# Performance work log

Hardware: AMD Instinct MI355X
Metric: run time of the kernel (lower is better)

Reference implementation:

```python
import jax, jax.numpy as jnp
import numpy as np

P_FACTOR = 3.0
EPS = 1e-12  # torch F.normalize eps


def _l2norm(x):
    # torch.nn.functional.normalize(x, dim=1): x / max(||x||_2, eps)
    n = jnp.sqrt(jnp.sum(x * x, axis=1, keepdims=True))
    return x / jnp.maximum(n, EPS)


def setup_inputs() -> dict:
    key = jax.random.key(0)
    k1, k2, k3, k4, k5 = jax.random.split(key, 5)
    B, N, D_IN, D_RED, C = 8192, 16384, 1024, 512, 28
    return {
        "features": jax.random.normal(k1, (B, D_IN), dtype=jnp.float32),
        "ex_features": jax.random.normal(k2, (N, D_IN), dtype=jnp.float32),
        "g_w": jax.random.normal(k3, (D_RED, D_IN), dtype=jnp.float32) * 0.02,
        "g_b": jax.random.normal(k4, (D_RED,), dtype=jnp.float32) * 0.02,
        "ex_classes": jax.random.uniform(k5, (N, C), dtype=jnp.float32),
    }


def reference(features, ex_features, g_w, g_b, ex_classes):
    # g: Linear(input_dim -> dim_reduce)
    f = features @ g_w.T + g_b          # [B, D_red]
    ef = ex_features @ g_w.T + g_b      # [N, D_red]
    # cosine similarity
    s = _l2norm(f) @ _l2norm(ef).T      # [B, N]
    # power-sign activation: |s|^p * sign(s)
    a = jnp.power(jnp.abs(s), P_FACTOR) * jnp.sign(s)
    echo = a @ ex_classes               # [B, C]
    b = jnp.clip(jnp.sum(ex_classes, axis=0), 1.0, None)
    echo = jnp.clip(echo / b, 0.0, 1.0)
    return echo
```

## Files before the change

kernel.cpp:

```cpp
#include <hip/hip_runtime.h>
#include <stdint.h>

typedef __attribute__((ext_vector_type(4))) float f32x4;
typedef __attribute__((ext_vector_type(8))) short s16x8;

#define MFMA16(A, B, C) __builtin_amdgcn_mfma_f32_16x16x32_bf16(A, B, C, 0, 0, 0)
#define WAIT_VM(N) asm volatile("s_waitcnt vmcnt(" #N ")" ::: "memory")
#define WAIT_LGKM() asm volatile("s_waitcnt lgkmcnt(0)" ::: "memory")
#define BAR() __builtin_amdgcn_s_barrier()
#define SCHED_FENCE() __builtin_amdgcn_sched_barrier(0)
#define SP1() __builtin_amdgcn_s_setprio(1)
#define SP0() __builtin_amdgcn_s_setprio(0)

#define PHASE_SYNC(N) do { SCHED_FENCE(); WAIT_LGKM(); WAIT_VM(N); BAR(); SCHED_FENCE(); } while (0)
#define PHASE_SYNC_NOVM() do { SCHED_FENCE(); WAIT_LGKM(); BAR(); SCHED_FENCE(); } while (0)

__device__ __forceinline__ unsigned short f2bf(float x) {
  union { float f; unsigned u; } v; v.f = x;
  return (unsigned short)((v.u + 0x7fffu + ((v.u >> 16) & 1u)) >> 16);
}

__global__ void k_cast_bf16(const float* __restrict__ in, unsigned short* __restrict__ out, int n4) {
  int i = blockIdx.x * blockDim.x + threadIdx.x;
  const int stride = gridDim.x * blockDim.x;
  for (; i < n4; i += stride) {
    const float4 v = ((const float4*)in)[i];
    ushort4 o;
    o.x = f2bf(v.x); o.y = f2bf(v.y); o.z = f2bf(v.z); o.w = f2bf(v.w);
    ((ushort4*)out)[i] = o;
  }
}

__global__ void k_excT(const float* __restrict__ exc, unsigned short* __restrict__ excT,
                       float* __restrict__ bvec) {
  const int c = blockIdx.x;
  const int tid = threadIdx.x;
  float sum = 0.f;
  for (int j = tid; j < 16384; j += 256) {
    const float v = (c < 28) ? exc[(size_t)j * 28 + c] : 0.f;
    excT[(size_t)c * 16384 + j] = f2bf(v);
    sum += v;
  }
  #pragma unroll
  for (int o = 32; o; o >>= 1) sum += __shfl_down(sum, o, 64);
  __shared__ float wsum[4];
  if ((tid & 63) == 0) wsum[tid >> 6] = sum;
  __syncthreads();
  if (tid == 0 && c < 28) bvec[c] = fmaxf(wsum[0] + wsum[1] + wsum[2] + wsum[3], 1.0f);
}

__device__ __forceinline__ void stage_a(const unsigned short* __restrict__ src, int ld,
                                        unsigned short* smem, int dsoff, int w, int offsrc) {
  #pragma unroll
  for (int c = 0; c < 4; ++c)
    __builtin_amdgcn_global_load_lds(
        (const __attribute__((address_space(1))) unsigned int*)(src + offsrc + c * 64 * ld),
        (__attribute__((address_space(3))) unsigned int*)(smem + dsoff + c * 4096 + w * 512),
        16, 0, 0);
}
__device__ __forceinline__ void stage_b(const unsigned short* __restrict__ src, int ld,
                                        unsigned short* smem, int dsoff, int w, int offsrc) {
  #pragma unroll
  for (int c = 0; c < 2; ++c)
    __builtin_amdgcn_global_load_lds(
        (const __attribute__((address_space(1))) unsigned int*)(src + offsrc + c * 64 * ld),
        (__attribute__((address_space(3))) unsigned int*)(smem + dsoff + c * 4096 + w * 512),
        16, 0, 0);
}

__device__ __forceinline__ void mma_step_p(const unsigned short* smem, int ao, int bo,
                                           int wr, int wc, int r, int q, f32x4 acc[8][2]) {
  const int rx = r & 7;
  #pragma unroll
  for (int ks = 0; ks < 2; ++ks) {
    const int sb = ((ks * 4 + q) ^ rx) << 3;
    s16x8 bf[2];
    #pragma unroll
    for (int j = 0; j < 2; ++j)
      bf[j] = *(const s16x8*)(smem + bo + (wc * 32 + j * 16 + r) * 64 + sb);
    #pragma unroll
    for (int i = 0; i < 8; ++i) {
      const s16x8 af = *(const s16x8*)(smem + ao + (wr * 128 + i * 16 + r) * 64 + sb);
      #pragma unroll
      for (int j = 0; j < 2; ++j)
        acc[i][j] = MFMA16(af, bf[j], acc[i][j]);
    }
  }
}

#define PA0 0
#define PB0 16384
#define PA1 24576
#define PB1 40960

__global__ __launch_bounds__(512, 2) void k_proj(const unsigned short* __restrict__ featbf,
                                                 const unsigned short* __restrict__ exbf,
                                                 const unsigned short* __restrict__ gwbf,
                                                 const float* __restrict__ gb,
                                                 float* __restrict__ fall) {
  __shared__ __align__(16) unsigned short smem[49152];
  const int tid = threadIdx.x, w = tid >> 6, lane = tid & 63;
  const int wr = w >> 2, wc = w & 3, r = lane & 15, q = lane >> 4;
  const int offsrc = (w * 8 + (lane >> 3)) * 1024 + (((lane & 7) ^ (lane >> 3)) << 3);
  const int m0 = blockIdx.x * 256;
  const int n0 = blockIdx.y * 128;
  const unsigned short* Asrc = (m0 < 8192) ? (featbf + (size_t)m0 * 1024)
                                           : (exbf + (size_t)(m0 - 8192) * 1024);
  const unsigned short* Bsrc = gwbf + (size_t)n0 * 1024;
  f32x4 acc[8][2];
  #pragma unroll
  for (int i = 0; i < 8; ++i)
    #pragma unroll
    for (int j = 0; j < 2; ++j) acc[i][j] = {0.f, 0.f, 0.f, 0.f};

  stage_a(Asrc, 1024, smem, PA0, w, offsrc);
  stage_b(Bsrc, 1024, smem, PB0, w, offsrc);
  for (int t = 0; t < 15; ++t) {
    const int na = ((t + 1) & 1) ? PA1 : PA0, nbb = ((t + 1) & 1) ? PB1 : PB0;
    stage_a(Asrc + (t + 1) * 64, 1024, smem, na, w, offsrc);
    stage_b(Bsrc + (t + 1) * 64, 1024, smem, nbb, w, offsrc);
    WAIT_VM(6);
    BAR();
    mma_step_p(smem, (t & 1) ? PA1 : PA0, (t & 1) ? PB1 : PB0, wr, wc, r, q, acc);
    WAIT_LGKM();
    BAR();
  }
  WAIT_VM(0);
  BAR();
  mma_step_p(smem, PA1, PB1, wr, wc, r, q, acc);

  #pragma unroll
  for (int j = 0; j < 2; ++j) {
    const int col = n0 + wc * 32 + j * 16 + r;
    const float bias = gb[col];
    #pragma unroll
    for (int i = 0; i < 8; ++i) {
      const int row0 = m0 + wr * 128 + i * 16 + q * 4;
      #pragma unroll
      for (int t = 0; t < 4; ++t)
        fall[(size_t)(row0 + t) * 512 + col] = acc[i][j][t] + bias;
    }
  }
}

__global__ __launch_bounds__(256) void k_norm(const float* __restrict__ fall,
                                              unsigned short* __restrict__ fn) {
  const int row = blockIdx.x * 4 + (threadIdx.x >> 6);
  const int lane = threadIdx.x & 63;
  const float4* p = (const float4*)(fall + (size_t)row * 512) + lane * 2;
  const float4 v0 = p[0], v1 = p[1];
  float ss = v0.x * v0.x + v0.y * v0.y + v0.z * v0.z + v0.w * v0.w
           + v1.x * v1.x + v1.y * v1.y + v1.z * v1.z + v1.w * v1.w;
  #pragma unroll
  for (int o = 32; o; o >>= 1) ss += __shfl_xor(ss, o, 64);
  const float sc = 1.0f / fmaxf(sqrtf(ss), 1e-12f);
  ushort4 o0, o1;
  o0.x = f2bf(v0.x * sc); o0.y = f2bf(v0.y * sc); o0.z = f2bf(v0.z * sc); o0.w = f2bf(v0.w * sc);
  o1.x = f2bf(v1.x * sc); o1.y = f2bf(v1.y * sc); o1.z = f2bf(v1.z * sc); o1.w = f2bf(v1.w * sc);
  ushort4* qo = (ushort4*)(fn + (size_t)row * 512) + lane * 2;
  qo[0] = o0; qo[1] = o1;
}

#define BUFSZ 32768
#define EXL 65536

__device__ __forceinline__ void stage_half(const unsigned short* __restrict__ src,
                                           unsigned short* smem, int dsoff, int tid) {
  const int rowh = tid >> 3;
  const unsigned short* g = src + (size_t)rowh * 512 + (((tid & 7) ^ (rowh & 7)) << 3);
  __builtin_amdgcn_global_load_lds(
      (const __attribute__((address_space(1))) unsigned int*)g,
      (__attribute__((address_space(3))) unsigned int*)(smem + dsoff + tid * 8), 16, 0, 0);
  __builtin_amdgcn_global_load_lds(
      (const __attribute__((address_space(1))) unsigned int*)(g + 64 * 512),
      (__attribute__((address_space(3))) unsigned int*)(smem + dsoff + 4096 + tid * 8), 16, 0, 0);
}

__device__ __forceinline__ void stage_exc(const unsigned short* __restrict__ excTg, int c0,
                                          unsigned short* smem, int tid) {
  const int row = tid >> 5, b = tid & 31;
  const int sb = ((b & 24) | ((b ^ (row & 7)) & 7)) << 3;
  const unsigned short* g = excTg + (size_t)row * 16384 + c0 + sb;
  __builtin_amdgcn_global_load_lds(
      (const __attribute__((address_space(1))) unsigned int*)g,
      (__attribute__((address_space(3))) unsigned int*)(smem + EXL + tid * 8), 16, 0, 0);
  __builtin_amdgcn_global_load_lds(
      (const __attribute__((address_space(1))) unsigned int*)(g + 16 * 16384),
      (__attribute__((address_space(3))) unsigned int*)(smem + EXL + 4096 + tid * 8), 16, 0, 0);
}

template<int MH, int NH>
__device__ __forceinline__ void mma_phase(const unsigned short* smem, int bufR,
                                          int wr, int wc, int r, int q, int rx,
                                          f32x4 acc[2][2][4][2]) {
  const unsigned short* A = smem + bufR + MH * 16384 + (wr * 64 + r) * 64;
  const unsigned short* B = smem + bufR + 8192 + NH * 16384 + (wc * 32 + r) * 64;
  const int s0 = (q ^ rx) << 3, s1 = ((4 + q) ^ rx) << 3;
  const s16x8 b00 = *(const s16x8*)(B + s0),        b01 = *(const s16x8*)(B + s1);
  const s16x8 b10 = *(const s16x8*)(B + 1024 + s0), b11 = *(const s16x8*)(B + 1024 + s1);
  #pragma unroll
  for (int fi = 0; fi < 4; ++fi) {
    const s16x8 a0 = *(const s16x8*)(A + fi * 1024 + s0);
    acc[MH][NH][fi][0] = MFMA16(a0, b00, acc[MH][NH][fi][0]);
    acc[MH][NH][fi][1] = MFMA16(a0, b10, acc[MH][NH][fi][1]);
    const s16x8 a1 = *(const s16x8*)(A + fi * 1024 + s1);
    acc[MH][NH][fi][0] = MFMA16(a1, b01, acc[MH][NH][fi][0]);
    acc[MH][NH][fi][1] = MFMA16(a1, b11, acc[MH][NH][fi][1]);
  }
}

__global__ __launch_bounds__(512, 2) void k_fused(const unsigned short* __restrict__ fnall,
                                                  const unsigned short* __restrict__ excT,
                                                  float* __restrict__ partial) {
  __shared__ __align__(16) unsigned short smem[73728];
  const int tid = threadIdx.x, w = tid >> 6, lane = tid & 63;
  const int wr = w >> 2, wc = w & 3, r = lane & 15, q = lane >> 4, rx = r & 7;
  const int r0 = blockIdx.x * 256;
  const int nchunk = blockIdx.y;
  const unsigned short* Abase = fnall + (size_t)r0 * 512;
  const unsigned short* Ebase = fnall + (size_t)8192 * 512;
  unsigned short* aLb = smem + BUFSZ;

  f32x4 acc[2][2][4][2];
  f32x4 eacc[2][2];
  #pragma unroll
  for (int a = 0; a < 2; ++a)
    #pragma unroll
    for (int b = 0; b < 2; ++b) eacc[a][b] = {0.f, 0.f, 0.f, 0.f};

  {
    const unsigned short* B0p = Ebase + (size_t)(nchunk * 4) * 256 * 512;
    stage_half(Abase, smem, 0, tid);
    stage_half(B0p, smem, 8192, tid);
    stage_half(Abase + 128 * 512, smem, 16384, tid);
    stage_half(B0p + 128 * 512, smem, 24576, tid);
  }

  for (int jt = 0; jt < 4; ++jt) {
    #pragma unroll
    for (int a = 0; a < 2; ++a)
      #pragma unroll
      for (int b = 0; b < 2; ++b)
        #pragma unroll
        for (int fi = 0; fi < 4; ++fi)
          #pragma unroll
          for (int fj = 0; fj < 2; ++fj) acc[a][b][fi][fj] = {0.f, 0.f, 0.f, 0.f};

    for (int tk = 0; tk < 8; ++tk) {
      const int kt = jt * 8 + tk;
      const int bufR = (kt & 1) * BUFSZ, bufW = bufR ^ BUFSZ;
      const int kn = (kt + 1) & 31;
      const unsigned short* An = Abase + (kn & 7) * 64;
      const unsigned short* Bn = Ebase + (size_t)((nchunk * 4 + (kn >> 3)) * 256) * 512 + (kn & 7) * 64;
      PHASE_SYNC(4);
      stage_half(An, smem, bufW + 0, tid);
      if (tk == 7) stage_exc(excT, (nchunk * 4 + jt) * 256, smem, tid);
      SP1(); mma_phase<0, 0>(smem, bufR, wr, wc, r, q, rx, acc); SP0();
      PHASE_SYNC(4);
      stage_half(Bn, smem, bufW + 8192, tid);
      SP1(); mma_phase<1, 0>(smem, bufR, wr, wc, r, q, rx, acc); SP0();
      PHASE_SYNC(4);
      stage_half(An + 128 * 512, smem, bufW + 16384, tid);
      SP1(); mma_phase<1, 1>(smem, bufR, wr, wc, r, q, rx, acc); SP0();
      PHASE_SYNC_NOVM();
      stage_half(Bn + 128 * 512, smem, bufW + 24576, tid);
      SP1(); mma_phase<0, 1>(smem, bufR, wr, wc, r, q, rx, acc); SP0();
    }

    const int c0 = (nchunk * 4 + jt) * 256;
    SCHED_FENCE(); WAIT_LGKM(); WAIT_VM(6); BAR(); SCHED_FENCE();
    #pragma unroll
    for (int h = 0; h < 2; ++h) {
      #pragma unroll
      for (int nh = 0; nh < 2; ++nh)
        #pragma unroll
        for (int fi = 0; fi < 4; ++fi)
          #pragma unroll
          for (int fj = 0; fj < 2; ++fj) {
            const int colc = nh * 128 + wc * 32 + fj * 16 + r;
            const int cb = colc >> 3, cl = colc & 7;
            #pragma unroll
            for (int t2 = 0; t2 < 4; ++t2) {
              const int row = wr * 64 + fi * 16 + q * 4 + t2;
              const float v = acc[h][nh][fi][fj][t2];
              aLb[row * 256 + ((((cb & 24) | ((cb ^ (row & 7)) & 7)) << 3) | cl)] = f2bf(v * v * v);
            }
          }
      SCHED_FENCE(); WAIT_LGKM(); BAR(); SCHED_FENCE();
      {
        const int rE = w * 16 + r;
        const int re8 = rE & 7;
        #pragma unroll
        for (int kc = 0; kc < 8; ++kc) {
          const int kb = kc * 4 + q;
          const s16x8 af = *(const s16x8*)(aLb + rE * 256 + (((kb & 24) | ((kb ^ re8) & 7)) << 3));
          #pragma unroll
          for (int nj = 0; nj < 2; ++nj) {
            const s16x8 bfr = *(const s16x8*)(smem + EXL + (nj * 16 + r) * 256 +
                                              (((kb & 24) | ((kb ^ rx) & 7)) << 3));
            eacc[h][nj] = MFMA16(af, bfr, eacc[h][nj]);
          }
        }
      }
      SCHED_FENCE(); WAIT_LGKM(); BAR(); SCHED_FENCE();
    }
  }

  #pragma unroll
  for (int h = 0; h < 2; ++h)
    #pragma unroll
    for (int nj = 0; nj < 2; ++nj) {
      const int rb = r0 + h * 128 + w * 16 + q * 4;
      const int cls = nj * 16 + r;
      #pragma unroll
      for (int t = 0; t < 4; ++t)
        partial[((size_t)nchunk * 8192 + rb + t) * 32 + cls] = eacc[h][nj][t];
    }
}

__global__ void k_reduce(const float* __restrict__ partial, const float* __restrict__ bvec,
                         float* __restrict__ out) {
  const int idx = blockIdx.x * 256 + threadIdx.x;
  const int row = idx / 28, c = idx - row * 28;
  float s = 0.f;
  #pragma unroll
  for (int nc = 0; nc < 16; ++nc) s += partial[((size_t)nc * 8192 + row) * 32 + c];
  out[idx] = fminf(fmaxf(s / bvec[c], 0.f), 1.f);
}

extern "C" void kernel_launch(void* const* d_in, const int* in_sizes, int n_in,
                              void* d_out, int out_size, void* d_ws, size_t ws_size,
                              hipStream_t stream) {
  const float* features    = (const float*)d_in[0];
  const float* ex_features = (const float*)d_in[1];
  const float* g_w         = (const float*)d_in[2];
  const float* g_b         = (const float*)d_in[3];
  const float* ex_classes  = (const float*)d_in[4];
  float* out = (float*)d_out;
  char* ws = (char*)d_ws;

  unsigned short* featbf = (unsigned short*)(ws + 0);
  unsigned short* exbf   = (unsigned short*)(ws + 16777216);
  unsigned short* fnall  = (unsigned short*)(ws + 0);
  float* fall            = (float*)(ws + 50331648);
  float* partial         = (float*)(ws + 50331648);
  unsigned short* gwbf   = (unsigned short*)(ws + 100663296);
  unsigned short* excT   = (unsigned short*)(ws + 101711872);
  float* bvec            = (float*)(ws + 102760448);

  k_cast_bf16<<<2048, 256, 0, stream>>>(features, featbf, 8192 * 1024 / 4);
  k_cast_bf16<<<2048, 256, 0, stream>>>(ex_features, exbf, 16384 * 1024 / 4);
  k_cast_bf16<<<512, 256, 0, stream>>>(g_w, gwbf, 512 * 1024 / 4);
  k_excT<<<32, 256, 0, stream>>>(ex_classes, excT, bvec);
  k_proj<<<dim3(96, 4), 512, 0, stream>>>(featbf, exbf, gwbf, g_b, fall);
  k_norm<<<6144, 256, 0, stream>>>(fall, fnall);
  k_fused<<<dim3(32, 16), 512, 0, stream>>>(fnall, excT, partial);
  k_reduce<<<896, 256, 0, stream>>>(partial, bvec, out);
}
```

Baseline: 255.6 us.

## Reorder MFMA quadrant phases to reuse A/B fragments across phases

Each k-step's four quadrant phases are reordered to (A0,B0), (A0,B1), (A1,B1), (A1,B0), and fragments now stay in registers between phases. This roughly halves LDS fragment reads per k-step. The async global-to-LDS staging order is permuted so each half-tile's write lands after its last read from the previous buffer. More fragment registers stay live alongside the large accumulator set, which risks spills or lower occupancy under the 512x2 launch bounds.

```diff
diff --git a/kernel.cpp b/kernel.cpp
--- a/kernel.cpp
+++ b/kernel.cpp
@@ -189,23 +189,31 @@
       (__attribute__((address_space(3))) unsigned int*)(smem + EXL + 4096 + tid * 8), 16, 0, 0);
 }
 
-template<int MH, int NH>
-__device__ __forceinline__ void mma_phase(const unsigned short* smem, int bufR,
-                                          int wr, int wc, int r, int q, int rx,
-                                          f32x4 acc[2][2][4][2]) {
+__device__ __forceinline__ void ld_a(const unsigned short* smem, int bufR, int MH,
+                                     int wr, int r, int s0, int s1, s16x8 a[4][2]) {
   const unsigned short* A = smem + bufR + MH * 16384 + (wr * 64 + r) * 64;
+  #pragma unroll
+  for (int fi = 0; fi < 4; ++fi) {
+    a[fi][0] = *(const s16x8*)(A + fi * 1024 + s0);
+    a[fi][1] = *(const s16x8*)(A + fi * 1024 + s1);
+  }
+}
+__device__ __forceinline__ void ld_b(const unsigned short* smem, int bufR, int NH,
+                                     int wc, int r, int s0, int s1, s16x8 b[2][2]) {
   const unsigned short* B = smem + bufR + 8192 + NH * 16384 + (wc * 32 + r) * 64;
-  const int s0 = (q ^ rx) << 3, s1 = ((4 + q) ^ rx) << 3;
-  const s16x8 b00 = *(const s16x8*)(B + s0),        b01 = *(const s16x8*)(B + s1);
-  const s16x8 b10 = *(const s16x8*)(B + 1024 + s0), b11 = *(const s16x8*)(B + 1024 + s1);
+  #pragma unroll
+  for (int j = 0; j < 2; ++j) {
+    b[j][0] = *(const s16x8*)(B + j * 1024 + s0);
+    b[j][1] = *(const s16x8*)(B + j * 1024 + s1);
+  }
+}
+__device__ __forceinline__ void mma_q(const s16x8 a[4][2], const s16x8 b[2][2], f32x4 accq[4][2]) {
   #pragma unroll
   for (int fi = 0; fi < 4; ++fi) {
-    const s16x8 a0 = *(const s16x8*)(A + fi * 1024 + s0);
-    acc[MH][NH][fi][0] = MFMA16(a0, b00, acc[MH][NH][fi][0]);
-    acc[MH][NH][fi][1] = MFMA16(a0, b10, acc[MH][NH][fi][1]);
-    const s16x8 a1 = *(const s16x8*)(A + fi * 1024 + s1);
-    acc[MH][NH][fi][0] = MFMA16(a1, b01, acc[MH][NH][fi][0]);
-    acc[MH][NH][fi][1] = MFMA16(a1, b11, acc[MH][NH][fi][1]);
+    accq[fi][0] = MFMA16(a[fi][0], b[0][0], accq[fi][0]);
+    accq[fi][1] = MFMA16(a[fi][0], b[1][0], accq[fi][1]);
+    accq[fi][0] = MFMA16(a[fi][1], b[0][1], accq[fi][0]);
+    accq[fi][1] = MFMA16(a[fi][1], b[1][1], accq[fi][1]);
   }
 }
 
@@ -215,6 +223,7 @@
   __shared__ __align__(16) unsigned short smem[73728];
   const int tid = threadIdx.x, w = tid >> 6, lane = tid & 63;
   const int wr = w >> 2, wc = w & 3, r = lane & 15, q = lane >> 4, rx = r & 7;
+  const int s0 = (q ^ rx) << 3, s1 = ((4 + q) ^ rx) << 3;
   const int r0 = blockIdx.x * 256;
   const int nchunk = blockIdx.y;
   const unsigned short* Abase = fnall + (size_t)r0 * 512;
@@ -232,8 +241,8 @@
     const unsigned short* B0p = Ebase + (size_t)(nchunk * 4) * 256 * 512;
     stage_half(Abase, smem, 0, tid);
     stage_half(B0p, smem, 8192, tid);
+    stage_half(B0p + 128 * 512, smem, 24576, tid);
     stage_half(Abase + 128 * 512, smem, 16384, tid);
-    stage_half(B0p + 128 * 512, smem, 24576, tid);
   }
 
   for (int jt = 0; jt < 4; ++jt) {
@@ -252,22 +261,34 @@
       const int kn = (kt + 1) & 31;
       const unsigned short* An = Abase + (kn & 7) * 64;
       const unsigned short* Bn = Ebase + (size_t)((nchunk * 4 + (kn >> 3)) * 256) * 512 + (kn & 7) * 64;
+      s16x8 afr[4][2], b0f[2][2], b1f[2][2];
       PHASE_SYNC(4);
       stage_half(An, smem, bufW + 0, tid);
       if (tk == 7) stage_exc(excT, (nchunk * 4 + jt) * 256, smem, tid);
-      SP1(); mma_phase<0, 0>(smem, bufR, wr, wc, r, q, rx, acc); SP0();
+      SP1();
+      ld_a(smem, bufR, 0, wr, r, s0, s1, afr);
+      ld_b(smem, bufR, 0, wc, r, s0, s1, b0f);
+      mma_q(afr, b0f, acc[0][0]);
+      SP0();
       PHASE_SYNC(4);
       stage_half(Bn, smem, bufW + 8192, tid);
-      SP1(); mma_phase<1, 0>(smem, bufR, wr, wc, r, q, rx, acc); SP0();
+      SP1();
+      ld_b(smem, bufR, 1, wc, r, s0, s1, b1f);
+      mma_q(afr, b1f, acc[0][1]);
+      SP0();
       PHASE_SYNC(4);
+      stage_half(Bn + 128 * 512, smem, bufW + 24576, tid);
+      SP1();
+      ld_a(smem, bufR, 1, wr, r, s0, s1, afr);
+      mma_q(afr, b1f, acc[1][1]);
+      SP0();
+      PHASE_SYNC_NOVM();
       stage_half(An + 128 * 512, smem, bufW + 16384, tid);
-      SP1(); mma_phase<1, 1>(smem, bufR, wr, wc, r, q, rx, acc); SP0();
-      PHASE_SYNC_NOVM();
-      stage_half(Bn + 128 * 512, smem, bufW + 24576, tid);
-      SP1(); mma_phase<0, 1>(smem, bufR, wr, wc, r, q, rx, acc); SP0();
-    }
-
-    const int c0 = (nchunk * 4 + jt) * 256;
+      SP1();
+      mma_q(afr, b0f, acc[1][0]);
+      SP0();
+    }
+
     SCHED_FENCE(); WAIT_LGKM(); WAIT_VM(6); BAR(); SCHED_FENCE();
     #pragma unroll
     for (int h = 0; h < 2; ++h) {
```

New measurement: 307.7 us. 20.4% more time.

## Switch main GEMM to 32x32x16 MFMA with quarter-K staging pipeline

Applied to the files above, without the earlier changes.

Replaces the 16x16x32 bf16 MFMA tiling of the similarity GEMM with 32x32x16 MFMAs, giving each wave a 128x64 sub-tile instead of split halves. The shared-memory staging is reorganized into four K-quarter stages per step, and the exc-table prefetch and next-column-chunk prefetch are peeled into a special last iteration with retuned vmcnt waits. The larger MFMA shape is meant to cut LDS read traffic per FLOP and instruction count. In exchange it drops the XOR swizzle, which risks LDS bank conflicts, and it adds more complex wait-count bookkeeping.

```diff
diff --git a/kernel.cpp b/kernel.cpp
--- a/kernel.cpp
+++ b/kernel.cpp
@@ -2,9 +2,11 @@
 #include <stdint.h>
 
 typedef __attribute__((ext_vector_type(4))) float f32x4;
+typedef __attribute__((ext_vector_type(16))) float f32x16;
 typedef __attribute__((ext_vector_type(8))) short s16x8;
 
 #define MFMA16(A, B, C) __builtin_amdgcn_mfma_f32_16x16x32_bf16(A, B, C, 0, 0, 0)
+#define MFMA32(A, B, C) __builtin_amdgcn_mfma_f32_32x32x16_bf16(A, B, C, 0, 0, 0)
 #define WAIT_VM(N) asm volatile("s_waitcnt vmcnt(" #N ")" ::: "memory")
 #define WAIT_LGKM() asm volatile("s_waitcnt lgkmcnt(0)" ::: "memory")
 #define BAR() __builtin_amdgcn_s_barrier()
@@ -13,7 +15,6 @@
 #define SP0() __builtin_amdgcn_s_setprio(0)
 
 #define PHASE_SYNC(N) do { SCHED_FENCE(); WAIT_LGKM(); WAIT_VM(N); BAR(); SCHED_FENCE(); } while (0)
-#define PHASE_SYNC_NOVM() do { SCHED_FENCE(); WAIT_LGKM(); BAR(); SCHED_FENCE(); } while (0)
 
 __device__ __forceinline__ unsigned short f2bf(float x) {
   union { float f; unsigned u; } v; v.f = x;
@@ -164,16 +165,12 @@
 #define BUFSZ 32768
 #define EXL 65536
 
-__device__ __forceinline__ void stage_half(const unsigned short* __restrict__ src,
-                                           unsigned short* smem, int dsoff, int tid) {
-  const int rowh = tid >> 3;
-  const unsigned short* g = src + (size_t)rowh * 512 + (((tid & 7) ^ (rowh & 7)) << 3);
+__device__ __forceinline__ void stage_q(const unsigned short* __restrict__ src,
+                                        unsigned short* smem, int dsoff, int tid) {
+  const unsigned short* g = src + (size_t)(tid >> 1) * 512 + (tid & 1) * 8;
   __builtin_amdgcn_global_load_lds(
       (const __attribute__((address_space(1))) unsigned int*)g,
       (__attribute__((address_space(3))) unsigned int*)(smem + dsoff + tid * 8), 16, 0, 0);
-  __builtin_amdgcn_global_load_lds(
-      (const __attribute__((address_space(1))) unsigned int*)(g + 64 * 512),
-      (__attribute__((address_space(3))) unsigned int*)(smem + dsoff + 4096 + tid * 8), 16, 0, 0);
 }
 
 __device__ __forceinline__ void stage_exc(const unsigned short* __restrict__ excTg, int c0,
@@ -189,39 +186,42 @@
       (__attribute__((address_space(3))) unsigned int*)(smem + EXL + 4096 + tid * 8), 16, 0, 0);
 }
 
-template<int MH, int NH>
-__device__ __forceinline__ void mma_phase(const unsigned short* smem, int bufR,
-                                          int wr, int wc, int r, int q, int rx,
-                                          f32x4 acc[2][2][4][2]) {
-  const unsigned short* A = smem + bufR + MH * 16384 + (wr * 64 + r) * 64;
-  const unsigned short* B = smem + bufR + 8192 + NH * 16384 + (wc * 32 + r) * 64;
-  const int s0 = (q ^ rx) << 3, s1 = ((4 + q) ^ rx) << 3;
-  const s16x8 b00 = *(const s16x8*)(B + s0),        b01 = *(const s16x8*)(B + s1);
-  const s16x8 b10 = *(const s16x8*)(B + 1024 + s0), b11 = *(const s16x8*)(B + 1024 + s1);
-  #pragma unroll
-  for (int fi = 0; fi < 4; ++fi) {
-    const s16x8 a0 = *(const s16x8*)(A + fi * 1024 + s0);
-    acc[MH][NH][fi][0] = MFMA16(a0, b00, acc[MH][NH][fi][0]);
-    acc[MH][NH][fi][1] = MFMA16(a0, b10, acc[MH][NH][fi][1]);
-    const s16x8 a1 = *(const s16x8*)(A + fi * 1024 + s1);
-    acc[MH][NH][fi][0] = MFMA16(a1, b01, acc[MH][NH][fi][0]);
-    acc[MH][NH][fi][1] = MFMA16(a1, b11, acc[MH][NH][fi][1]);
-  }
-}
+template<int P>
+__device__ __forceinline__ void mma_phase32(const unsigned short* smem, int bufR,
+                                            int wr, int wc, int l31, int hs8, f32x16 acc[4][2]) {
+  const unsigned short* Aq = smem + bufR + P * 4096;
+  const unsigned short* Bq = smem + bufR + 16384 + P * 4096;
+  const s16x8 bf0 = *(const s16x8*)(Bq + (wc * 64 + l31) * 16 + hs8);
+  const s16x8 bf1 = *(const s16x8*)(Bq + (wc * 64 + 32 + l31) * 16 + hs8);
+  #pragma unroll
+  for (int rt = 0; rt < 4; ++rt) {
+    const s16x8 af = *(const s16x8*)(Aq + (wr * 128 + rt * 32 + l31) * 16 + hs8);
+    acc[rt][0] = MFMA32(af, bf0, acc[rt][0]);
+    acc[rt][1] = MFMA32(af, bf1, acc[rt][1]);
+  }
+}
+
+#define STAGE_PAIR(P)                                                     \
+  do {                                                                    \
+    stage_q(An + (P) * 16, smem, bufW + (P) * 4096, tid);                 \
+    stage_q(Bn + (P) * 16, smem, bufW + 16384 + (P) * 4096, tid);         \
+  } while (0)
 
 __global__ __launch_bounds__(512, 2) void k_fused(const unsigned short* __restrict__ fnall,
                                                   const unsigned short* __restrict__ excT,
                                                   float* __restrict__ partial) {
   __shared__ __align__(16) unsigned short smem[73728];
   const int tid = threadIdx.x, w = tid >> 6, lane = tid & 63;
-  const int wr = w >> 2, wc = w & 3, r = lane & 15, q = lane >> 4, rx = r & 7;
+  const int wr = w >> 2, wc = w & 3;
+  const int l31 = lane & 31, hs = lane >> 5, hs8 = hs * 8;
+  const int r = lane & 15, q = lane >> 4, rx = r & 7;
   const int r0 = blockIdx.x * 256;
   const int nchunk = blockIdx.y;
   const unsigned short* Abase = fnall + (size_t)r0 * 512;
   const unsigned short* Ebase = fnall + (size_t)8192 * 512;
   unsigned short* aLb = smem + BUFSZ;
 
-  f32x4 acc[2][2][4][2];
+  f32x16 acc[4][2];
   f32x4 eacc[2][2];
   #pragma unroll
   for (int a = 0; a < 2; ++a)
@@ -229,63 +229,82 @@
     for (int b = 0; b < 2; ++b) eacc[a][b] = {0.f, 0.f, 0.f, 0.f};
 
   {
-    const unsigned short* B0p = Ebase + (size_t)(nchunk * 4) * 256 * 512;
-    stage_half(Abase, smem, 0, tid);
-    stage_half(B0p, smem, 8192, tid);
-    stage_half(Abase + 128 * 512, smem, 16384, tid);
-    stage_half(B0p + 128 * 512, smem, 24576, tid);
+    const unsigned short* An = Abase;
+    const unsigned short* Bn = Ebase + (size_t)(nchunk * 4) * 256 * 512;
+    const int bufW = 0;
+    STAGE_PAIR(0); STAGE_PAIR(1); STAGE_PAIR(2); STAGE_PAIR(3);
   }
 
   for (int jt = 0; jt < 4; ++jt) {
     #pragma unroll
-    for (int a = 0; a < 2; ++a)
+    for (int rt = 0; rt < 4; ++rt)
       #pragma unroll
-      for (int b = 0; b < 2; ++b)
+      for (int ct = 0; ct < 2; ++ct)
         #pragma unroll
-        for (int fi = 0; fi < 4; ++fi)
-          #pragma unroll
-          for (int fj = 0; fj < 2; ++fj) acc[a][b][fi][fj] = {0.f, 0.f, 0.f, 0.f};
-
-    for (int tk = 0; tk < 8; ++tk) {
+        for (int e = 0; e < 16; ++e) acc[rt][ct][e] = 0.f;
+
+    for (int tk = 0; tk < 7; ++tk) {
       const int kt = jt * 8 + tk;
       const int bufR = (kt & 1) * BUFSZ, bufW = bufR ^ BUFSZ;
-      const int kn = (kt + 1) & 31;
+      const int kn = kt + 1;
       const unsigned short* An = Abase + (kn & 7) * 64;
       const unsigned short* Bn = Ebase + (size_t)((nchunk * 4 + (kn >> 3)) * 256) * 512 + (kn & 7) * 64;
-      PHASE_SYNC(4);
-      stage_half(An, smem, bufW + 0, tid);
-      if (tk == 7) stage_exc(excT, (nchunk * 4 + jt) * 256, smem, tid);
-      SP1(); mma_phase<0, 0>(smem, bufR, wr, wc, r, q, rx, acc); SP0();
-      PHASE_SYNC(4);
-      stage_half(Bn, smem, bufW + 8192, tid);
-      SP1(); mma_phase<1, 0>(smem, bufR, wr, wc, r, q, rx, acc); SP0();
-      PHASE_SYNC(4);
-      stage_half(An + 128 * 512, smem, bufW + 16384, tid);
-      SP1(); mma_phase<1, 1>(smem, bufR, wr, wc, r, q, rx, acc); SP0();
-      PHASE_SYNC_NOVM();
-      stage_half(Bn + 128 * 512, smem, bufW + 24576, tid);
-      SP1(); mma_phase<0, 1>(smem, bufR, wr, wc, r, q, rx, acc); SP0();
-    }
-
+      PHASE_SYNC(6); STAGE_PAIR(0);
+      SP1(); mma_phase32<0>(smem, bufR, wr, wc, l31, hs8, acc); SP0();
+      PHASE_SYNC(6); STAGE_PAIR(1);
+      SP1(); mma_phase32<1>(smem, bufR, wr, wc, l31, hs8, acc); SP0();
+      PHASE_SYNC(6); STAGE_PAIR(2);
+      SP1(); mma_phase32<2>(smem, bufR, wr, wc, l31, hs8, acc); SP0();
+      PHASE_SYNC(6); STAGE_PAIR(3);
+      SP1(); mma_phase32<3>(smem, bufR, wr, wc, l31, hs8, acc); SP0();
+    }
+    {
+      const int bufR = BUFSZ, bufW = 0;
+      const int c0e = (nchunk * 4 + jt) * 256;
+      const unsigned short* An = Abase;
+      const unsigned short* Bn = Ebase + (size_t)((nchunk * 4 + jt + 1) * 256) * 512;
+      if (jt < 3) {
+        PHASE_SYNC(6); stage_exc(excT, c0e, smem, tid); STAGE_PAIR(0);
+        SP1(); mma_phase32<0>(smem, bufR, wr, wc, l31, hs8, acc); SP0();
+        PHASE_SYNC(8); STAGE_PAIR(1);
+        SP1(); mma_phase32<1>(smem, bufR, wr, wc, l31, hs8, acc); SP0();
+        PHASE_SYNC(8); STAGE_PAIR(2);
+        SP1(); mma_phase32<2>(smem, bufR, wr, wc, l31, hs8, acc); SP0();
+        PHASE_SYNC(8); STAGE_PAIR(3);
+        SP1(); mma_phase32<3>(smem, bufR, wr, wc, l31, hs8, acc); SP0();
+      } else {
+        PHASE_SYNC(6); stage_exc(excT, c0e, smem, tid);
+        SP1(); mma_phase32<0>(smem, bufR, wr, wc, l31, hs8, acc); SP0();
+        PHASE_SYNC(6);
+        SP1(); mma_phase32<1>(smem, bufR, wr, wc, l31, hs8, acc); SP0();
+        PHASE_SYNC(4);
+        SP1(); mma_phase32<2>(smem, bufR, wr, wc, l31, hs8, acc); SP0();
+        PHASE_SYNC(2);
+        SP1(); mma_phase32<3>(smem, bufR, wr, wc, l31, hs8, acc); SP0();
+      }
+    }
+
+    SCHED_FENCE(); WAIT_LGKM();
+    if (jt < 3) { WAIT_VM(8); } else { WAIT_VM(0); }
+    BAR(); SCHED_FENCE();
     const int c0 = (nchunk * 4 + jt) * 256;
-    SCHED_FENCE(); WAIT_LGKM(); WAIT_VM(6); BAR(); SCHED_FENCE();
+    (void)c0;
     #pragma unroll
     for (int h = 0; h < 2; ++h) {
-      #pragma unroll
-      for (int nh = 0; nh < 2; ++nh)
+      if (wr == h) {
         #pragma unroll
-        for (int fi = 0; fi < 4; ++fi)
+        for (int rt = 0; rt < 4; ++rt)
           #pragma unroll
-          for (int fj = 0; fj < 2; ++fj) {
-            const int colc = nh * 128 + wc * 32 + fj * 16 + r;
-            const int cb = colc >> 3, cl = colc & 7;
+          for (int ct = 0; ct < 2; ++ct)
             #pragma unroll
-            for (int t2 = 0; t2 < 4; ++t2) {
-              const int row = wr * 64 + fi * 16 + q * 4 + t2;
-              const float v = acc[h][nh][fi][fj][t2];
-              aLb[row * 256 + ((((cb & 24) | ((cb ^ (row & 7)) & 7)) << 3) | cl)] = f2bf(v * v * v);
+            for (int e = 0; e < 16; ++e) {
+              const int rh = rt * 32 + (e & 3) + 8 * (e >> 2) + 4 * hs;
+              const int c = wc * 64 + ct * 32 + l31;
+              const int cb = c >> 3, cl = c & 7;
+              const float v = acc[rt][ct][e];
+              aLb[rh * 256 + ((((cb & 24) | ((cb ^ (rh & 7)) & 7)) << 3) | cl)] = f2bf(v * v * v);
             }
-          }
+      }
       SCHED_FENCE(); WAIT_LGKM(); BAR(); SCHED_FENCE();
       {
         const int rE = w * 16 + r;
```

New measurement: 947.8 us. +270.8%, slower.

## Restructure main GEMM pipeline to K=32 tiles with simple double buffering

Applied to the files above, without the earlier changes.

Replaces the 4-phase K=64 quarter-staged pipeline with a plain double-buffered loop over K=32 tiles. Each iteration issues full A and B tile loads, then runs all MFMAs for the tile. The unswizzled LDS layout shrinks shared memory use. This trades finer overlap for fewer barriers, but adds full vmcnt(0) waits each step and risks LDS bank conflicts from the 64-byte row stride without swizzle.

```diff
diff --git a/kernel.cpp b/kernel.cpp
--- a/kernel.cpp
+++ b/kernel.cpp
@@ -11,9 +11,6 @@
 #define SCHED_FENCE() __builtin_amdgcn_sched_barrier(0)
 #define SP1() __builtin_amdgcn_s_setprio(1)
 #define SP0() __builtin_amdgcn_s_setprio(0)
-
-#define PHASE_SYNC(N) do { SCHED_FENCE(); WAIT_LGKM(); WAIT_VM(N); BAR(); SCHED_FENCE(); } while (0)
-#define PHASE_SYNC_NOVM() do { SCHED_FENCE(); WAIT_LGKM(); BAR(); SCHED_FENCE(); } while (0)
 
 __device__ __forceinline__ unsigned short f2bf(float x) {
   union { float f; unsigned u; } v; v.f = x;
@@ -161,19 +158,16 @@
   qo[0] = o0; qo[1] = o1;
 }
 
-#define BUFSZ 32768
-#define EXL 65536
-
-__device__ __forceinline__ void stage_half(const unsigned short* __restrict__ src,
-                                           unsigned short* smem, int dsoff, int tid) {
-  const int rowh = tid >> 3;
-  const unsigned short* g = src + (size_t)rowh * 512 + (((tid & 7) ^ (rowh & 7)) << 3);
+#define BUF 16384
+#define EXLo 32768
+#define ALo 40960
+
+__device__ __forceinline__ void stage_p(const unsigned short* __restrict__ src,
+                                        unsigned short* smem, int dsoff, int tid) {
+  const unsigned short* g = src + (size_t)(tid >> 2) * 512 + (tid & 3) * 8;
   __builtin_amdgcn_global_load_lds(
       (const __attribute__((address_space(1))) unsigned int*)g,
       (__attribute__((address_space(3))) unsigned int*)(smem + dsoff + tid * 8), 16, 0, 0);
-  __builtin_amdgcn_global_load_lds(
-      (const __attribute__((address_space(1))) unsigned int*)(g + 64 * 512),
-      (__attribute__((address_space(3))) unsigned int*)(smem + dsoff + 4096 + tid * 8), 16, 0, 0);
 }
 
 __device__ __forceinline__ void stage_exc(const unsigned short* __restrict__ excTg, int c0,
@@ -183,29 +177,34 @@
   const unsigned short* g = excTg + (size_t)row * 16384 + c0 + sb;
   __builtin_amdgcn_global_load_lds(
       (const __attribute__((address_space(1))) unsigned int*)g,
-      (__attribute__((address_space(3))) unsigned int*)(smem + EXL + tid * 8), 16, 0, 0);
+      (__attribute__((address_space(3))) unsigned int*)(smem + EXLo + tid * 8), 16, 0, 0);
   __builtin_amdgcn_global_load_lds(
       (const __attribute__((address_space(1))) unsigned int*)(g + 16 * 16384),
-      (__attribute__((address_space(3))) unsigned int*)(smem + EXL + 4096 + tid * 8), 16, 0, 0);
-}
-
-template<int MH, int NH>
-__device__ __forceinline__ void mma_phase(const unsigned short* smem, int bufR,
-                                          int wr, int wc, int r, int q, int rx,
-                                          f32x4 acc[2][2][4][2]) {
-  const unsigned short* A = smem + bufR + MH * 16384 + (wr * 64 + r) * 64;
-  const unsigned short* B = smem + bufR + 8192 + NH * 16384 + (wc * 32 + r) * 64;
-  const int s0 = (q ^ rx) << 3, s1 = ((4 + q) ^ rx) << 3;
-  const s16x8 b00 = *(const s16x8*)(B + s0),        b01 = *(const s16x8*)(B + s1);
-  const s16x8 b10 = *(const s16x8*)(B + 1024 + s0), b11 = *(const s16x8*)(B + 1024 + s1);
-  #pragma unroll
-  for (int fi = 0; fi < 4; ++fi) {
-    const s16x8 a0 = *(const s16x8*)(A + fi * 1024 + s0);
-    acc[MH][NH][fi][0] = MFMA16(a0, b00, acc[MH][NH][fi][0]);
-    acc[MH][NH][fi][1] = MFMA16(a0, b10, acc[MH][NH][fi][1]);
-    const s16x8 a1 = *(const s16x8*)(A + fi * 1024 + s1);
-    acc[MH][NH][fi][0] = MFMA16(a1, b01, acc[MH][NH][fi][0]);
-    acc[MH][NH][fi][1] = MFMA16(a1, b11, acc[MH][NH][fi][1]);
+      (__attribute__((address_space(3))) unsigned int*)(smem + EXLo + 4096 + tid * 8), 16, 0, 0);
+}
+
+__device__ __forceinline__ void ktile32(const unsigned short* smem, int bufR,
+                                        int wr, int wc, int r, int q, f32x4 acc[2][2][4][2]) {
+  const int koff = q * 8;
+  const unsigned short* Bb = smem + bufR + 8192 + (wc * 32 + r) * 32 + koff;
+  s16x8 bf[2][2];
+  #pragma unroll
+  for (int nh = 0; nh < 2; ++nh)
+    #pragma unroll
+    for (int fj = 0; fj < 2; ++fj)
+      bf[nh][fj] = *(const s16x8*)(Bb + (nh * 128 + fj * 16) * 32);
+  #pragma unroll
+  for (int MH = 0; MH < 2; ++MH) {
+    const unsigned short* Ab = smem + bufR + (MH * 128 + wr * 64 + r) * 32 + koff;
+    #pragma unroll
+    for (int fi = 0; fi < 4; ++fi) {
+      const s16x8 af = *(const s16x8*)(Ab + fi * 512);
+      #pragma unroll
+      for (int nh = 0; nh < 2; ++nh)
+        #pragma unroll
+        for (int fj = 0; fj < 2; ++fj)
+          acc[MH][nh][fi][fj] = MFMA16(af, bf[nh][fj], acc[MH][nh][fi][fj]);
+    }
   }
 }
 
@@ -219,7 +218,7 @@
   const int nchunk = blockIdx.y;
   const unsigned short* Abase = fnall + (size_t)r0 * 512;
   const unsigned short* Ebase = fnall + (size_t)8192 * 512;
-  unsigned short* aLb = smem + BUFSZ;
+  unsigned short* aLb = smem + ALo;
 
   f32x4 acc[2][2][4][2];
   f32x4 eacc[2][2];
@@ -229,14 +228,16 @@
     for (int b = 0; b < 2; ++b) eacc[a][b] = {0.f, 0.f, 0.f, 0.f};
 
   {
-    const unsigned short* B0p = Ebase + (size_t)(nchunk * 4) * 256 * 512;
-    stage_half(Abase, smem, 0, tid);
-    stage_half(B0p, smem, 8192, tid);
-    stage_half(Abase + 128 * 512, smem, 16384, tid);
-    stage_half(B0p + 128 * 512, smem, 24576, tid);
+    const unsigned short* Bp = Ebase + (size_t)(nchunk * 4) * 256 * 512;
+    stage_p(Bp, smem, 8192, tid);
+    stage_p(Bp + 128 * 512, smem, 12288, tid);
+    stage_p(Abase, smem, 0, tid);
+    stage_p(Abase + 128 * 512, smem, 4096, tid);
   }
 
   for (int jt = 0; jt < 4; ++jt) {
+    const int c0 = (nchunk * 4 + jt) * 256;
+    const unsigned short* Bsrc = Ebase + (size_t)c0 * 512;
     #pragma unroll
     for (int a = 0; a < 2; ++a)
       #pragma unroll
@@ -246,29 +247,32 @@
           #pragma unroll
           for (int fj = 0; fj < 2; ++fj) acc[a][b][fi][fj] = {0.f, 0.f, 0.f, 0.f};
 
-    for (int tk = 0; tk < 8; ++tk) {
-      const int kt = jt * 8 + tk;
-      const int bufR = (kt & 1) * BUFSZ, bufW = bufR ^ BUFSZ;
-      const int kn = (kt + 1) & 31;
-      const unsigned short* An = Abase + (kn & 7) * 64;
-      const unsigned short* Bn = Ebase + (size_t)((nchunk * 4 + (kn >> 3)) * 256) * 512 + (kn & 7) * 64;
-      PHASE_SYNC(4);
-      stage_half(An, smem, bufW + 0, tid);
-      if (tk == 7) stage_exc(excT, (nchunk * 4 + jt) * 256, smem, tid);
-      SP1(); mma_phase<0, 0>(smem, bufR, wr, wc, r, q, rx, acc); SP0();
-      PHASE_SYNC(4);
-      stage_half(Bn, smem, bufW + 8192, tid);
-      SP1(); mma_phase<1, 0>(smem, bufR, wr, wc, r, q, rx, acc); SP0();
-      PHASE_SYNC(4);
-      stage_half(An + 128 * 512, smem, bufW + 16384, tid);
-      SP1(); mma_phase<1, 1>(smem, bufR, wr, wc, r, q, rx, acc); SP0();
-      PHASE_SYNC_NOVM();
-      stage_half(Bn + 128 * 512, smem, bufW + 24576, tid);
-      SP1(); mma_phase<0, 1>(smem, bufR, wr, wc, r, q, rx, acc); SP0();
-    }
-
-    const int c0 = (nchunk * 4 + jt) * 256;
-    SCHED_FENCE(); WAIT_LGKM(); WAIT_VM(6); BAR(); SCHED_FENCE();
+    for (int tk = 0; tk < 16; ++tk) {
+      const int bufR = (tk & 1) * BUF, bufW = bufR ^ BUF;
+      SCHED_FENCE(); WAIT_LGKM(); WAIT_VM(0); BAR(); SCHED_FENCE();
+      if (tk < 15) {
+        const unsigned short* An = Abase + (tk + 1) * 32;
+        const unsigned short* Bn = Bsrc + (tk + 1) * 32;
+        stage_p(Bn, smem, bufW + 8192, tid);
+        stage_p(Bn + 128 * 512, smem, bufW + 12288, tid);
+        stage_p(An, smem, bufW + 0, tid);
+        stage_p(An + 128 * 512, smem, bufW + 4096, tid);
+      } else {
+        stage_exc(excT, c0, smem, tid);
+        if (jt < 3) {
+          const unsigned short* Bn = Ebase + (size_t)(c0 + 256) * 512;
+          stage_p(Bn, smem, bufW + 8192, tid);
+          stage_p(Bn + 128 * 512, smem, bufW + 12288, tid);
+          stage_p(Abase, smem, bufW + 0, tid);
+          stage_p(Abase + 128 * 512, smem, bufW + 4096, tid);
+        }
+      }
+      SP1(); ktile32(smem, bufR, wr, wc, r, q, acc); SP0();
+    }
+
+    SCHED_FENCE(); WAIT_LGKM();
+    if (jt < 3) { WAIT_VM(4); } else { WAIT_VM(0); }
+    BAR(); SCHED_FENCE();
     #pragma unroll
     for (int h = 0; h < 2; ++h) {
       #pragma unroll
@@ -296,7 +300,7 @@
           const s16x8 af = *(const s16x8*)(aLb + rE * 256 + (((kb & 24) | ((kb ^ re8) & 7)) << 3));
           #pragma unroll
           for (int nj = 0; nj < 2; ++nj) {
-            const s16x8 bfr = *(const s16x8*)(smem + EXL + (nj * 16 + r) * 256 +
+            const s16x8 bfr = *(const s16x8*)(smem + EXLo + (nj * 16 + r) * 256 +
                                               (((kb & 24) | ((kb ^ rx) & 7)) << 3));
             eacc[h][nj] = MFMA16(af, bfr, eacc[h][nj]);
           }
```

New measurement: 250.2 us. 1.02x faster.
